# Performance work log

Measured on AMD Instinct MI355X. Metric: run time of the kernel, lower is better.

## Reference

```python
import jax, jax.numpy as jnp
import numpy as np
from jax import lax

N_IN = 200000
N_OUT = 400000
K3 = 27
M = 100000
C_IN = 128
C_OUT = 128
EPS = 1e-5


def setup_inputs() -> dict:
    key = jax.random.key(0)
    k1, k2, k3, k4 = jax.random.split(key, 4)
    feats = jax.random.normal(k1, (N_IN, C_IN), dtype=jnp.float32)
    W = jax.random.normal(k2, (K3, C_IN, C_OUT), dtype=jnp.float32) * (1.0 / np.sqrt(C_IN))
    gamma = jnp.ones((C_OUT,), dtype=jnp.float32)
    beta = jnp.zeros((C_OUT,), dtype=jnp.float32)
    in_maps = jax.random.randint(k3, (K3, M), 0, N_IN, dtype=jnp.int32)
    out_maps = jax.random.randint(k4, (K3, M), 0, N_OUT, dtype=jnp.int32)
    return {"feats": feats, "W": W, "gamma": gamma, "beta": beta,
            "in_maps": in_maps, "out_maps": out_maps, "n_out": N_OUT}


def sparse_conv_transpose(feats, W, in_maps, out_maps, n_out):
    # gather-GEMM-scatter over K3 kernel offsets (fixed small set -> scan)
    out0 = jnp.zeros((n_out, W.shape[-1]), dtype=feats.dtype)

    def body(out, xs):
        im, om, Wk = xs                      # [M], [M], [C_in, C_out]
        contrib = feats[im] @ Wk             # gather [M, C_in] -> GEMM -> [M, C_out]
        return out.at[om].add(contrib), None  # scatter-add

    out, _ = lax.scan(body, out0, (in_maps, out_maps, W))
    return out


def reference(feats, W, gamma, beta, in_maps, out_maps, n_out):
    out = sparse_conv_transpose(feats, W, in_maps, out_maps, n_out)  # [N_out, C_out]
    # MinkowskiBatchNorm (training mode): per-channel stats over all points
    mean = jnp.mean(out, axis=0)
    var = jnp.var(out, axis=0)
    y = (out - mean) * lax.rsqrt(var + EPS) * gamma + beta
    return y
```

## Files before the change

### kernel.cpp

```cpp
#include <hip/hip_runtime.h>

#define K3c    27
#define Mc     100000
#define NINc   200000
#define NOUTc  400000
#define Cc     128
#define EPSc   1e-5f

#define NBUCK  6250
#define NCNT   (K3c * NBUCK)
#define BPK    391
#define CPK    1563

#define WS_STATS   0u
#define WS_COUNTS  4096u
#define WS_SIM     1048576u
#define WS_SOM     12582912u
#define WS_WFH     25165824u
#define WS_WFL     26214400u

typedef __attribute__((ext_vector_type(8))) short short8;
typedef __attribute__((ext_vector_type(4))) float f32x4;

__device__ inline unsigned fbits(float f) { return __builtin_bit_cast(unsigned, f); }
__device__ inline float bfloat(unsigned u) { return __builtin_bit_cast(float, u); }

__device__ inline unsigned pack_hi2(float f0, float f1) {
    return (fbits(f0) >> 16) | (fbits(f1) & 0xFFFF0000u);
}
__device__ inline float trunc_bf16_f(float f) { return bfloat(fbits(f) & 0xFFFF0000u); }

__device__ inline unsigned short bf16_rne(float f) {
    unsigned u = fbits(f);
    u += 0x7FFFu + ((u >> 16) & 1u);
    return (unsigned short)(u >> 16);
}

__global__ __launch_bounds__(256) void zero_kernel(float4* __restrict__ out4,
                                                   float* __restrict__ ws_stats,
                                                   unsigned* __restrict__ counts) {
    const int n4 = NOUTc * (Cc / 4);
    const int stride = gridDim.x * blockDim.x;
    int idx = blockIdx.x * blockDim.x + threadIdx.x;
    const float4 z = make_float4(0.f, 0.f, 0.f, 0.f);
    for (int i = idx; i < n4; i += stride) out4[i] = z;
    for (int i = idx; i < NCNT; i += stride) counts[i] = 0u;
    if (idx < 512) ws_stats[idx] = 0.f;
}

__global__ __launch_bounds__(256) void wprep_kernel(const float* __restrict__ W,
                                                    short8* __restrict__ wfh,
                                                    short8* __restrict__ wfl) {
    int tid = blockIdx.x * 256 + threadIdx.x;
    int k     = tid >> 11;
    int rem   = tid & 2047;
    int kstep = rem >> 9;
    int cb    = (rem >> 6) & 7;
    int lane  = rem & 63;
    int n   = cb * 16 + (lane & 15);
    int kk0 = kstep * 32 + (lane >> 4) * 8;
    const float* src = W + k * (Cc * Cc) + kk0 * Cc + n;
    short8 h, l;
#pragma unroll
    for (int j = 0; j < 8; ++j) {
        float f = src[j * Cc];
        unsigned short hb = bf16_rne(f);
        h[j] = (short)hb;
        float hf = bfloat(((unsigned)hb) << 16);
        l[j] = (short)bf16_rne(f - hf);
    }
    wfh[tid] = h;
    wfl[tid] = l;
}

__global__ __launch_bounds__(256) void hist_kernel(const int* __restrict__ out_maps,
                                                   unsigned* __restrict__ counts) {
    int b = blockIdx.x;
    int k = b / BPK;
    int m = (b - k * BPK) * 256 + threadIdx.x;
    if (m < Mc) {
        int om = out_maps[k * Mc + m];
        atomicAdd(&counts[k * NBUCK + (om >> 6)], 1u);
    }
}

__global__ __launch_bounds__(1024) void scan_kernel(unsigned* __restrict__ counts) {
    __shared__ unsigned lds[1024];
    const int t = threadIdx.x;
    const int CHUNK = 165;
    int base = t * CHUNK;
    unsigned s = 0;
    for (int j = 0; j < CHUNK; ++j) {
        int i = base + j;
        if (i < NCNT) s += counts[i];
    }
    lds[t] = s;
    __syncthreads();
    for (int off = 1; off < 1024; off <<= 1) {
        unsigned v = (t >= off) ? lds[t - off] : 0u;
        __syncthreads();
        lds[t] += v;
        __syncthreads();
    }
    unsigned run = lds[t] - s;
    for (int j = 0; j < CHUNK; ++j) {
        int i = base + j;
        if (i < NCNT) {
            unsigned c = counts[i];
            counts[i] = run;
            run += c;
        }
    }
}

__global__ __launch_bounds__(256) void build_kernel(const int* __restrict__ in_maps,
                                                    const int* __restrict__ out_maps,
                                                    unsigned* __restrict__ offs,
                                                    int* __restrict__ sorted_im,
                                                    int* __restrict__ sorted_om) {
    int b = blockIdx.x;
    int k = b / BPK;
    int m = (b - k * BPK) * 256 + threadIdx.x;
    if (m < Mc) {
        int om = out_maps[k * Mc + m];
        int im = in_maps[k * Mc + m];
        unsigned pos = atomicAdd(&offs[k * NBUCK + (om >> 6)], 1u);
        sorted_im[pos] = im;
        sorted_om[pos] = om;
    }
}

__global__ __launch_bounds__(256) void gemm_scatter_kernel(
    const float* __restrict__ feats,
    const short8* __restrict__ wfh, const short8* __restrict__ wfl,
    const int* __restrict__ sorted_im, const int* __restrict__ sorted_om,
    float* __restrict__ out)
{
    __shared__ short fsh[64 * 136];
    __shared__ short fsl[64 * 136];

    const int t = threadIdx.x;
    const int bx = blockIdx.x;
    const int k = bx / CPK;
    const int c = bx - k * CPK;
    const int pairbase = k * Mc + c * 64;
    const int valid = min(64, Mc - c * 64);

    {
        const int r = t >> 2;
        const int cg = t & 3;
        const bool ok = (r < valid);
        long im = ok ? (long)sorted_im[pairbase + r] : 0;
        const float4* src4 = (const float4*)(feats + im * Cc + cg * 32);
        unsigned* fh32 = (unsigned*)fsh;
        unsigned* fl32 = (unsigned*)fsl;
#pragma unroll
        for (int j = 0; j < 8; ++j) {
            float4 v = ok ? src4[j] : make_float4(0.f, 0.f, 0.f, 0.f);
            int col = cg * 32 + j * 4;
            int idx = r * 68 + (col >> 1);
            fh32[idx]     = pack_hi2(v.x, v.y);
            fh32[idx + 1] = pack_hi2(v.z, v.w);
            float lx = v.x - trunc_bf16_f(v.x);
            float ly = v.y - trunc_bf16_f(v.y);
            float lz = v.z - trunc_bf16_f(v.z);
            float lw = v.w - trunc_bf16_f(v.w);
            fl32[idx]     = pack_hi2(lx, ly);
            fl32[idx + 1] = pack_hi2(lz, lw);
        }
    }
    __syncthreads();

    const int wave = t >> 6;
    const int lane = t & 63;
    const int m    = lane & 15;
    const int quad = lane >> 4;

    f32x4 acc[8];
#pragma unroll
    for (int cb = 0; cb < 8; ++cb) acc[cb] = (f32x4){0.f, 0.f, 0.f, 0.f};

    const int arow = wave * 16 + m;
    for (int kstep = 0; kstep < 4; ++kstep) {
        const short* ah = fsh + arow * 136 + kstep * 32 + quad * 8;
        const short* al = fsl + arow * 136 + kstep * 32 + quad * 8;
        short8 a_hi = *(const short8*)ah;
        short8 a_lo = *(const short8*)al;
        int fb = ((k * 4 + kstep) * 8) * 64 + lane;
#pragma unroll
        for (int cb = 0; cb < 8; ++cb) {
            short8 b_hi = wfh[fb + cb * 64];
            short8 b_lo = wfl[fb + cb * 64];
            acc[cb] = __builtin_amdgcn_mfma_f32_16x16x32_bf16(a_hi, b_hi, acc[cb], 0, 0, 0);
            acc[cb] = __builtin_amdgcn_mfma_f32_16x16x32_bf16(a_lo, b_hi, acc[cb], 0, 0, 0);
            acc[cb] = __builtin_amdgcn_mfma_f32_16x16x32_bf16(a_hi, b_lo, acc[cb], 0, 0, 0);
        }
    }

    const int rbase = wave * 16 + quad * 4;
#pragma unroll
    for (int reg = 0; reg < 4; ++reg) {
        int row = rbase + reg;
        if (row < valid) {
            long om = (long)sorted_om[pairbase + row];
            float* dst = out + om * Cc + m;
#pragma unroll
            for (int cb = 0; cb < 8; ++cb)
                unsafeAtomicAdd(dst + cb * 16, acc[cb][reg]);
        }
    }
}

__global__ __launch_bounds__(256) void stats_kernel(const float4* __restrict__ out4,
                                                    float* __restrict__ stats) {
    const int t  = threadIdx.x;
    const int tx = t & 31;
    const int ty = t >> 5;

    float4 s = make_float4(0.f, 0.f, 0.f, 0.f);
    float4 q = make_float4(0.f, 0.f, 0.f, 0.f);
    int row0 = blockIdx.x * 400 + ty;
    for (int j = 0; j < 50; ++j) {
        float4 v = out4[(row0 + j * 8) * 32 + tx];
        s.x += v.x; s.y += v.y; s.z += v.z; s.w += v.w;
        q.x += v.x * v.x; q.y += v.y * v.y; q.z += v.z * v.z; q.w += v.w * v.w;
    }

    __shared__ float4 redS[256];
    __shared__ float4 redQ[256];
    redS[t] = s; redQ[t] = q;
    __syncthreads();
    if (ty == 0) {
#pragma unroll
        for (int jj = 1; jj < 8; ++jj) {
            float4 o = redS[jj * 32 + tx];
            s.x += o.x; s.y += o.y; s.z += o.z; s.w += o.w;
            float4 oq = redQ[jj * 32 + tx];
            q.x += oq.x; q.y += oq.y; q.z += oq.z; q.w += oq.w;
        }
        unsafeAtomicAdd(&stats[tx * 4 + 0], s.x);
        unsafeAtomicAdd(&stats[tx * 4 + 1], s.y);
        unsafeAtomicAdd(&stats[tx * 4 + 2], s.z);
        unsafeAtomicAdd(&stats[tx * 4 + 3], s.w);
        unsafeAtomicAdd(&stats[Cc + tx * 4 + 0], q.x);
        unsafeAtomicAdd(&stats[Cc + tx * 4 + 1], q.y);
        unsafeAtomicAdd(&stats[Cc + tx * 4 + 2], q.z);
        unsafeAtomicAdd(&stats[Cc + tx * 4 + 3], q.w);
    }
}

__global__ void finalize_kernel(const float* __restrict__ gamma,
                                const float* __restrict__ beta,
                                float* __restrict__ stats) {
    int c = threadIdx.x;
    float inv_n = 1.0f / (float)NOUTc;
    float mean = stats[c] * inv_n;
    float var  = stats[Cc + c] * inv_n - mean * mean;
    float scale = gamma[c] * rsqrtf(var + EPSc);
    stats[2 * Cc + c] = scale;
    stats[3 * Cc + c] = beta[c] - mean * scale;
}

__global__ __launch_bounds__(256) void norm_kernel(float4* __restrict__ out4,
                                                   const float* __restrict__ stats) {
    const float4* stats4 = (const float4*)stats;
    int idx0 = blockIdx.x * blockDim.x + threadIdx.x;
    int c4 = idx0 & 31;
    float4 sc = stats4[64 + c4];
    float4 sh = stats4[96 + c4];
    const int n4 = NOUTc * (Cc / 4);
    const int stride = gridDim.x * blockDim.x;
    for (int i = idx0; i < n4; i += stride) {
        float4 v = out4[i];
        v.x = v.x * sc.x + sh.x;
        v.y = v.y * sc.y + sh.y;
        v.z = v.z * sc.z + sh.z;
        v.w = v.w * sc.w + sh.w;
        out4[i] = v;
    }
}

extern "C" void kernel_launch(void* const* d_in, const int* in_sizes, int n_in,
                              void* d_out, int out_size, void* d_ws, size_t ws_size,
                              hipStream_t stream) {
    const float* feats    = (const float*)d_in[0];
    const float* W        = (const float*)d_in[1];
    const float* gamma    = (const float*)d_in[2];
    const float* beta     = (const float*)d_in[3];
    const int*   in_maps  = (const int*)d_in[4];
    const int*   out_maps = (const int*)d_in[5];
    float* out = (float*)d_out;

    char* ws = (char*)d_ws;
    float*    stats     = (float*)(ws + WS_STATS);
    unsigned* counts    = (unsigned*)(ws + WS_COUNTS);
    int*      sorted_im = (int*)(ws + WS_SIM);
    int*      sorted_om = (int*)(ws + WS_SOM);
    short8*   wfh       = (short8*)(ws + WS_WFH);
    short8*   wfl       = (short8*)(ws + WS_WFL);

    zero_kernel<<<4096, 256, 0, stream>>>((float4*)out, stats, counts);
    wprep_kernel<<<216, 256, 0, stream>>>(W, wfh, wfl);
    hist_kernel<<<K3c * BPK, 256, 0, stream>>>(out_maps, counts);
    scan_kernel<<<1, 1024, 0, stream>>>(counts);
    build_kernel<<<K3c * BPK, 256, 0, stream>>>(in_maps, out_maps, counts,
                                                sorted_im, sorted_om);
    gemm_scatter_kernel<<<K3c * CPK, 256, 0, stream>>>(feats, wfh, wfl,
                                                       sorted_im, sorted_om, out);
    stats_kernel<<<1000, 256, 0, stream>>>((const float4*)out, stats);
    finalize_kernel<<<1, 128, 0, stream>>>(gamma, beta, stats);
    norm_kernel<<<4096, 256, 0, stream>>>((float4*)out, stats);
}
```

Baseline: 2.319 ms.

## Bucket pairs by output tile, accumulate in LDS, fuse stats into gemm

Reorders the counting-sort key to bucket-major (output tile of 64 rows, then kernel offset), so each block owns one 64-row output tile. All contributions for that tile accumulate via workgroup-scope LDS atomics, and the tile is written once. This removes the zeroing of the output, the global float atomics and the separate stats pass, which is folded into the block epilogue. Features are gathered straight from global memory into registers, and im, k and the row are packed into one 32-bit word. The cost is uneven per-block work, only 6250 blocks, and wave-level dynamic scheduling over the 27 offsets with partially filled 16-row MFMA tiles.

```diff
diff --git a/kernel.cpp b/kernel.cpp
--- a/kernel.cpp
+++ b/kernel.cpp
@@ -8,14 +8,12 @@
 #define EPSc   1e-5f
 
 #define NBUCK  6250
-#define NCNT   (K3c * NBUCK)
+#define NCNT   (NBUCK * K3c)
 #define BPK    391
-#define CPK    1563
 
 #define WS_STATS   0u
 #define WS_COUNTS  4096u
-#define WS_SIM     1048576u
-#define WS_SOM     12582912u
+#define WS_SPK     1048576u
 #define WS_WFH     25165824u
 #define WS_WFL     26214400u
 
@@ -24,11 +22,6 @@
 
 __device__ inline unsigned fbits(float f) { return __builtin_bit_cast(unsigned, f); }
 __device__ inline float bfloat(unsigned u) { return __builtin_bit_cast(float, u); }
-
-__device__ inline unsigned pack_hi2(float f0, float f1) {
-    return (fbits(f0) >> 16) | (fbits(f1) & 0xFFFF0000u);
-}
-__device__ inline float trunc_bf16_f(float f) { return bfloat(fbits(f) & 0xFFFF0000u); }
 
 __device__ inline unsigned short bf16_rne(float f) {
     unsigned u = fbits(f);
@@ -36,16 +29,15 @@
     return (unsigned short)(u >> 16);
 }
 
-__global__ __launch_bounds__(256) void zero_kernel(float4* __restrict__ out4,
-                                                   float* __restrict__ ws_stats,
-                                                   unsigned* __restrict__ counts) {
-    const int n4 = NOUTc * (Cc / 4);
-    const int stride = gridDim.x * blockDim.x;
-    int idx = blockIdx.x * blockDim.x + threadIdx.x;
-    const float4 z = make_float4(0.f, 0.f, 0.f, 0.f);
-    for (int i = idx; i < n4; i += stride) out4[i] = z;
-    for (int i = idx; i < NCNT; i += stride) counts[i] = 0u;
-    if (idx < 512) ws_stats[idx] = 0.f;
+#define SPLIT1(F, H, L) { unsigned hb_ = fbits(F) & 0xFFFF0000u; \
+                          (H) = (short)(hb_ >> 16); \
+                          (L) = (short)(fbits((F) - bfloat(hb_)) >> 16); }
+
+__global__ __launch_bounds__(256) void zero2_kernel(float* __restrict__ stats,
+                                                    unsigned* __restrict__ counts) {
+    int idx = blockIdx.x * 256 + threadIdx.x;
+    if (idx < NCNT) counts[idx] = 0u;
+    if (idx < 512) stats[idx] = 0.f;
 }
 
 __global__ __launch_bounds__(256) void wprep_kernel(const float* __restrict__ W,
@@ -73,14 +65,14 @@
     wfl[tid] = l;
 }
 
-__global__ __launch_bounds__(256) void hist_kernel(const int* __restrict__ out_maps,
-                                                   unsigned* __restrict__ counts) {
+__global__ __launch_bounds__(256) void hist2_kernel(const int* __restrict__ out_maps,
+                                                    unsigned* __restrict__ counts) {
     int b = blockIdx.x;
     int k = b / BPK;
     int m = (b - k * BPK) * 256 + threadIdx.x;
     if (m < Mc) {
         int om = out_maps[k * Mc + m];
-        atomicAdd(&counts[k * NBUCK + (om >> 6)], 1u);
+        atomicAdd(&counts[(unsigned)(om >> 6) * 27u + (unsigned)k], 1u);
     }
 }
 
@@ -113,139 +105,164 @@
     }
 }
 
-__global__ __launch_bounds__(256) void build_kernel(const int* __restrict__ in_maps,
-                                                    const int* __restrict__ out_maps,
-                                                    unsigned* __restrict__ offs,
-                                                    int* __restrict__ sorted_im,
-                                                    int* __restrict__ sorted_om) {
+__global__ __launch_bounds__(256) void build2_kernel(const int* __restrict__ in_maps,
+                                                     const int* __restrict__ out_maps,
+                                                     unsigned* __restrict__ offs,
+                                                     unsigned* __restrict__ sorted_pk) {
     int b = blockIdx.x;
     int k = b / BPK;
     int m = (b - k * BPK) * 256 + threadIdx.x;
     if (m < Mc) {
         int om = out_maps[k * Mc + m];
         int im = in_maps[k * Mc + m];
-        unsigned pos = atomicAdd(&offs[k * NBUCK + (om >> 6)], 1u);
-        sorted_im[pos] = im;
-        sorted_om[pos] = om;
-    }
-}
-
-__global__ __launch_bounds__(256) void gemm_scatter_kernel(
+        unsigned pos = atomicAdd(&offs[(unsigned)(om >> 6) * 27u + (unsigned)k], 1u);
+        sorted_pk[pos] = (unsigned)im | ((unsigned)k << 18) | ((unsigned)(om & 63) << 23);
+    }
+}
+
+__global__ __launch_bounds__(256, 4) void gemm2_kernel(
     const float* __restrict__ feats,
     const short8* __restrict__ wfh, const short8* __restrict__ wfl,
-    const int* __restrict__ sorted_im, const int* __restrict__ sorted_om,
-    float* __restrict__ out)
+    const unsigned* __restrict__ counts,
+    const unsigned* __restrict__ sorted_pk,
+    float* __restrict__ out, float* __restrict__ stats)
 {
-    __shared__ short fsh[64 * 136];
-    __shared__ short fsl[64 * 136];
-
+    __shared__ float accs[64 * Cc];
+    __shared__ unsigned earr[28];
+    __shared__ int kctr;
+    __shared__ float sred[Cc], qred[Cc];
+
+    const int b = blockIdx.x;
     const int t = threadIdx.x;
-    const int bx = blockIdx.x;
-    const int k = bx / CPK;
-    const int c = bx - k * CPK;
-    const int pairbase = k * Mc + c * 64;
-    const int valid = min(64, Mc - c * 64);
-
+
+    if (t < 27) earr[t + 1] = counts[b * 27 + t];
+    if (t == 27) earr[0] = (b == 0) ? 0u : counts[b * 27 - 1];
+    if (t == 28) kctr = 0;
     {
-        const int r = t >> 2;
-        const int cg = t & 3;
-        const bool ok = (r < valid);
-        long im = ok ? (long)sorted_im[pairbase + r] : 0;
-        const float4* src4 = (const float4*)(feats + im * Cc + cg * 32);
-        unsigned* fh32 = (unsigned*)fsh;
-        unsigned* fl32 = (unsigned*)fsl;
-#pragma unroll
-        for (int j = 0; j < 8; ++j) {
-            float4 v = ok ? src4[j] : make_float4(0.f, 0.f, 0.f, 0.f);
-            int col = cg * 32 + j * 4;
-            int idx = r * 68 + (col >> 1);
-            fh32[idx]     = pack_hi2(v.x, v.y);
-            fh32[idx + 1] = pack_hi2(v.z, v.w);
-            float lx = v.x - trunc_bf16_f(v.x);
-            float ly = v.y - trunc_bf16_f(v.y);
-            float lz = v.z - trunc_bf16_f(v.z);
-            float lw = v.w - trunc_bf16_f(v.w);
-            fl32[idx]     = pack_hi2(lx, ly);
-            fl32[idx + 1] = pack_hi2(lz, lw);
-        }
+        f32x4* a4 = (f32x4*)accs;
+        const f32x4 z = {0.f, 0.f, 0.f, 0.f};
+#pragma unroll
+        for (int i = 0; i < 8; ++i) a4[t + i * 256] = z;
     }
     __syncthreads();
 
-    const int wave = t >> 6;
     const int lane = t & 63;
     const int m    = lane & 15;
     const int quad = lane >> 4;
 
-    f32x4 acc[8];
-#pragma unroll
-    for (int cb = 0; cb < 8; ++cb) acc[cb] = (f32x4){0.f, 0.f, 0.f, 0.f};
-
-    const int arow = wave * 16 + m;
-    for (int kstep = 0; kstep < 4; ++kstep) {
-        const short* ah = fsh + arow * 136 + kstep * 32 + quad * 8;
-        const short* al = fsl + arow * 136 + kstep * 32 + quad * 8;
-        short8 a_hi = *(const short8*)ah;
-        short8 a_lo = *(const short8*)al;
-        int fb = ((k * 4 + kstep) * 8) * 64 + lane;
-#pragma unroll
-        for (int cb = 0; cb < 8; ++cb) {
-            short8 b_hi = wfh[fb + cb * 64];
-            short8 b_lo = wfl[fb + cb * 64];
-            acc[cb] = __builtin_amdgcn_mfma_f32_16x16x32_bf16(a_hi, b_hi, acc[cb], 0, 0, 0);
-            acc[cb] = __builtin_amdgcn_mfma_f32_16x16x32_bf16(a_lo, b_hi, acc[cb], 0, 0, 0);
-            acc[cb] = __builtin_amdgcn_mfma_f32_16x16x32_bf16(a_hi, b_lo, acc[cb], 0, 0, 0);
-        }
-    }
-
-    const int rbase = wave * 16 + quad * 4;
-#pragma unroll
-    for (int reg = 0; reg < 4; ++reg) {
-        int row = rbase + reg;
-        if (row < valid) {
-            long om = (long)sorted_om[pairbase + row];
-            float* dst = out + om * Cc + m;
-#pragma unroll
-            for (int cb = 0; cb < 8; ++cb)
-                unsafeAtomicAdd(dst + cb * 16, acc[cb][reg]);
-        }
-    }
-}
-
-__global__ __launch_bounds__(256) void stats_kernel(const float4* __restrict__ out4,
-                                                    float* __restrict__ stats) {
-    const int t  = threadIdx.x;
-    const int tx = t & 31;
-    const int ty = t >> 5;
-
-    float4 s = make_float4(0.f, 0.f, 0.f, 0.f);
-    float4 q = make_float4(0.f, 0.f, 0.f, 0.f);
-    int row0 = blockIdx.x * 400 + ty;
-    for (int j = 0; j < 50; ++j) {
-        float4 v = out4[(row0 + j * 8) * 32 + tx];
-        s.x += v.x; s.y += v.y; s.z += v.z; s.w += v.w;
-        q.x += v.x * v.x; q.y += v.y * v.y; q.z += v.z * v.z; q.w += v.w * v.w;
-    }
-
-    __shared__ float4 redS[256];
-    __shared__ float4 redQ[256];
-    redS[t] = s; redQ[t] = q;
+    for (;;) {
+        int kk = 0;
+        if (lane == 0) kk = atomicAdd(&kctr, 1);
+        kk = __shfl(kk, 0);
+        if (kk >= K3c) break;
+        const unsigned sk = earr[kk];
+        const unsigned ek = earr[kk + 1];
+        for (unsigned p0 = sk; p0 < ek; p0 += 32) {
+            const int nA = (int)(ek - p0);
+            const int n0 = nA < 16 ? nA : 16;
+            int n1 = nA - 16; n1 = n1 < 0 ? 0 : (n1 > 16 ? 16 : n1);
+            const bool two = (n1 > 0);
+
+            unsigned pk0 = (m < n0) ? sorted_pk[p0 + m] : 0u;
+            unsigned pk1 = (two && m < n1) ? sorted_pk[p0 + 16 + m] : 0u;
+            const float* ap0 = feats + (long)(pk0 & 0x3FFFFu) * Cc + quad * 8;
+            const float* ap1 = feats + (long)(pk1 & 0x3FFFFu) * Cc + quad * 8;
+
+            f32x4 acc0[8], acc1[8];
+            const f32x4 z = {0.f, 0.f, 0.f, 0.f};
+#pragma unroll
+            for (int cb = 0; cb < 8; ++cb) { acc0[cb] = z; acc1[cb] = z; }
+
+            for (int kstep = 0; kstep < 4; ++kstep) {
+                short8 a0h, a0l, a1h, a1l;
+                {
+                    float4 v0 = *(const float4*)(ap0 + kstep * 32);
+                    float4 v1 = *(const float4*)(ap0 + kstep * 32 + 4);
+                    SPLIT1(v0.x, a0h[0], a0l[0]); SPLIT1(v0.y, a0h[1], a0l[1]);
+                    SPLIT1(v0.z, a0h[2], a0l[2]); SPLIT1(v0.w, a0h[3], a0l[3]);
+                    SPLIT1(v1.x, a0h[4], a0l[4]); SPLIT1(v1.y, a0h[5], a0l[5]);
+                    SPLIT1(v1.z, a0h[6], a0l[6]); SPLIT1(v1.w, a0h[7], a0l[7]);
+                }
+                if (two) {
+                    float4 v0 = *(const float4*)(ap1 + kstep * 32);
+                    float4 v1 = *(const float4*)(ap1 + kstep * 32 + 4);
+                    SPLIT1(v0.x, a1h[0], a1l[0]); SPLIT1(v0.y, a1h[1], a1l[1]);
+                    SPLIT1(v0.z, a1h[2], a1l[2]); SPLIT1(v0.w, a1h[3], a1l[3]);
+                    SPLIT1(v1.x, a1h[4], a1l[4]); SPLIT1(v1.y, a1h[5], a1l[5]);
+                    SPLIT1(v1.z, a1h[6], a1l[6]); SPLIT1(v1.w, a1h[7], a1l[7]);
+                }
+                const int fb = ((kk * 4 + kstep) * 8) * 64 + lane;
+#pragma unroll
+                for (int cb = 0; cb < 8; ++cb) {
+                    short8 bh = wfh[fb + cb * 64];
+                    short8 bl = wfl[fb + cb * 64];
+                    acc0[cb] = __builtin_amdgcn_mfma_f32_16x16x32_bf16(a0h, bh, acc0[cb], 0, 0, 0);
+                    acc0[cb] = __builtin_amdgcn_mfma_f32_16x16x32_bf16(a0l, bh, acc0[cb], 0, 0, 0);
+                    acc0[cb] = __builtin_amdgcn_mfma_f32_16x16x32_bf16(a0h, bl, acc0[cb], 0, 0, 0);
+                    if (two) {
+                        acc1[cb] = __builtin_amdgcn_mfma_f32_16x16x32_bf16(a1h, bh, acc1[cb], 0, 0, 0);
+                        acc1[cb] = __builtin_amdgcn_mfma_f32_16x16x32_bf16(a1l, bh, acc1[cb], 0, 0, 0);
+                        acc1[cb] = __builtin_amdgcn_mfma_f32_16x16x32_bf16(a1h, bl, acc1[cb], 0, 0, 0);
+                    }
+                }
+            }
+
+#pragma unroll
+            for (int reg = 0; reg < 4; ++reg) {
+                const int prow = quad * 4 + reg;
+                unsigned pks = (unsigned)__shfl((int)pk0, prow);
+                if (prow < n0) {
+                    float* dst = accs + ((pks >> 23) & 63u) * Cc + m;
+#pragma unroll
+                    for (int cb = 0; cb < 8; ++cb)
+                        __hip_atomic_fetch_add(dst + cb * 16, acc0[cb][reg],
+                                               __ATOMIC_RELAXED, __HIP_MEMORY_SCOPE_WORKGROUP);
+                }
+            }
+            if (two) {
+#pragma unroll
+                for (int reg = 0; reg < 4; ++reg) {
+                    const int prow = quad * 4 + reg;
+                    unsigned pks = (unsigned)__shfl((int)pk1, prow);
+                    if (prow < n1) {
+                        float* dst = accs + ((pks >> 23) & 63u) * Cc + m;
+#pragma unroll
+                        for (int cb = 0; cb < 8; ++cb)
+                            __hip_atomic_fetch_add(dst + cb * 16, acc1[cb][reg],
+                                                   __ATOMIC_RELAXED, __HIP_MEMORY_SCOPE_WORKGROUP);
+                    }
+                }
+            }
+        }
+    }
     __syncthreads();
-    if (ty == 0) {
-#pragma unroll
-        for (int jj = 1; jj < 8; ++jj) {
-            float4 o = redS[jj * 32 + tx];
-            s.x += o.x; s.y += o.y; s.z += o.z; s.w += o.w;
-            float4 oq = redQ[jj * 32 + tx];
-            q.x += oq.x; q.y += oq.y; q.z += oq.z; q.w += oq.w;
-        }
-        unsafeAtomicAdd(&stats[tx * 4 + 0], s.x);
-        unsafeAtomicAdd(&stats[tx * 4 + 1], s.y);
-        unsafeAtomicAdd(&stats[tx * 4 + 2], s.z);
-        unsafeAtomicAdd(&stats[tx * 4 + 3], s.w);
-        unsafeAtomicAdd(&stats[Cc + tx * 4 + 0], q.x);
-        unsafeAtomicAdd(&stats[Cc + tx * 4 + 1], q.y);
-        unsafeAtomicAdd(&stats[Cc + tx * 4 + 2], q.z);
-        unsafeAtomicAdd(&stats[Cc + tx * 4 + 3], q.w);
+
+    {
+        const int c4 = t & 31;
+        const int rg = t >> 5;
+        float4* dst4 = (float4*)(out + (long)b * 64 * Cc);
+        const float4* a4 = (const float4*)accs;
+#pragma unroll
+        for (int i = 0; i < 8; ++i) {
+            const int r = rg * 8 + i;
+            dst4[r * 32 + c4] = a4[r * 32 + c4];
+        }
+    }
+    {
+        const int col  = t & 127;
+        const int half = t >> 7;
+        float s = 0.f, q = 0.f;
+        for (int r = half * 32; r < half * 32 + 32; ++r) {
+            float v = accs[r * Cc + col];
+            s += v; q += v * v;
+        }
+        if (half) { sred[col] = s; qred[col] = q; }
+        __syncthreads();
+        if (!half) {
+            s += sred[col]; q += qred[col];
+            unsafeAtomicAdd(&stats[col], s);
+            unsafeAtomicAdd(&stats[Cc + col], q);
+        }
     }
 }
 
@@ -294,20 +311,16 @@
     char* ws = (char*)d_ws;
     float*    stats     = (float*)(ws + WS_STATS);
     unsigned* counts    = (unsigned*)(ws + WS_COUNTS);
-    int*      sorted_im = (int*)(ws + WS_SIM);
-    int*      sorted_om = (int*)(ws + WS_SOM);
+    unsigned* sorted_pk = (unsigned*)(ws + WS_SPK);
     short8*   wfh       = (short8*)(ws + WS_WFH);
     short8*   wfl       = (short8*)(ws + WS_WFL);
 
-    zero_kernel<<<4096, 256, 0, stream>>>((float4*)out, stats, counts);
+    zero2_kernel<<<660, 256, 0, stream>>>(stats, counts);
     wprep_kernel<<<216, 256, 0, stream>>>(W, wfh, wfl);
-    hist_kernel<<<K3c * BPK, 256, 0, stream>>>(out_maps, counts);
+    hist2_kernel<<<K3c * BPK, 256, 0, stream>>>(out_maps, counts);
     scan_kernel<<<1, 1024, 0, stream>>>(counts);
-    build_kernel<<<K3c * BPK, 256, 0, stream>>>(in_maps, out_maps, counts,
-                                                sorted_im, sorted_om);
-    gemm_scatter_kernel<<<K3c * CPK, 256, 0, stream>>>(feats, wfh, wfl,
-                                                       sorted_im, sorted_om, out);
-    stats_kernel<<<1000, 256, 0, stream>>>((const float4*)out, stats);
+    build2_kernel<<<K3c * BPK, 256, 0, stream>>>(in_maps, out_maps, counts, sorted_pk);
+    gemm2_kernel<<<NBUCK, 256, 0, stream>>>(feats, wfh, wfl, counts, sorted_pk, out, stats);
     finalize_kernel<<<1, 128, 0, stream>>>(gamma, beta, stats);
     norm_kernel<<<4096, 256, 0, stream>>>((float4*)out, stats);
 }
```

Measured after the change: 2.784 ms. 1.2x slower.

## Replace atomic scatter-add with sorted contribution buffer and per-output segmented reduction

Applied to the files above, without the earlier changes.

The GEMM kernel now writes each row's contribution to a slot in a staging buffer, using a second counting sort keyed by output row. A separate kernel then sums each output row's contributions and writes the result with plain stores. This removes the float atomics into the output and the full zeroing of the output. In exchange it adds a global histogram and scan over 400k rows, extra staging traffic (fp16 when workspace is small, which loses precision), and work split into slabs with many more launches.

```diff
diff --git a/kernel.cpp b/kernel.cpp
--- a/kernel.cpp
+++ b/kernel.cpp
@@ -1,4 +1,5 @@
 #include <hip/hip_runtime.h>
+#include <hip/hip_fp16.h>
 
 #define K3c    27
 #define Mc     100000
@@ -8,16 +9,22 @@
 #define EPSc   1e-5f
 
 #define NBUCK  6250
-#define NCNT   (K3c * NBUCK)
+#define NCNTA  (K3c * NBUCK)
+#define NCNTG  NOUTc
 #define BPK    391
-#define CPK    1563
+#define SCANBA 165
+#define SCANBG 391
 
 #define WS_STATS   0u
-#define WS_COUNTS  4096u
-#define WS_SIM     1048576u
-#define WS_SOM     12582912u
-#define WS_WFH     25165824u
-#define WS_WFL     26214400u
+#define WS_CNTA    4096u
+#define WS_AUXA    679936u
+#define WS_CNTG    681984u
+#define WS_AUXG    2282496u
+#define WS_WFH     2285568u
+#define WS_WFL     3170304u
+#define WS_SIMA    4055040u
+#define WS_PGA     14855040u
+#define WS_CBUF    25657344u
 
 typedef __attribute__((ext_vector_type(8))) short short8;
 typedef __attribute__((ext_vector_type(4))) float f32x4;
@@ -36,16 +43,19 @@
     return (unsigned short)(u >> 16);
 }
 
-__global__ __launch_bounds__(256) void zero_kernel(float4* __restrict__ out4,
-                                                   float* __restrict__ ws_stats,
-                                                   unsigned* __restrict__ counts) {
-    const int n4 = NOUTc * (Cc / 4);
-    const int stride = gridDim.x * blockDim.x;
-    int idx = blockIdx.x * blockDim.x + threadIdx.x;
-    const float4 z = make_float4(0.f, 0.f, 0.f, 0.f);
-    for (int i = idx; i < n4; i += stride) out4[i] = z;
-    for (int i = idx; i < NCNT; i += stride) counts[i] = 0u;
-    if (idx < 512) ws_stats[idx] = 0.f;
+__device__ inline unsigned short f2h(float f) { return __half_as_ushort(__float2half(f)); }
+__device__ inline float h2f(unsigned short u) { return __half2float(__ushort_as_half(u)); }
+
+__device__ inline void storeC(unsigned short* p, float v) { *p = f2h(v); }
+__device__ inline void storeC(float* p, float v) { *p = v; }
+
+__global__ __launch_bounds__(256) void zero3_kernel(float* __restrict__ stats,
+                                                    unsigned* __restrict__ cntA,
+                                                    unsigned* __restrict__ cntG) {
+    int idx = blockIdx.x * 256 + threadIdx.x;
+    if (idx < NCNTA) cntA[idx] = 0u;
+    if (idx < NCNTG) cntG[idx] = 0u;
+    if (idx < 512) stats[idx] = 0.f;
 }
 
 __global__ __launch_bounds__(256) void wprep_kernel(const float* __restrict__ W,
@@ -73,84 +83,107 @@
     wfl[tid] = l;
 }
 
-__global__ __launch_bounds__(256) void hist_kernel(const int* __restrict__ out_maps,
-                                                   unsigned* __restrict__ counts) {
+__global__ __launch_bounds__(256) void hist3_kernel(const int* __restrict__ out_maps,
+                                                    unsigned* __restrict__ cntA,
+                                                    unsigned* __restrict__ cntG) {
     int b = blockIdx.x;
     int k = b / BPK;
     int m = (b - k * BPK) * 256 + threadIdx.x;
     if (m < Mc) {
         int om = out_maps[k * Mc + m];
-        atomicAdd(&counts[k * NBUCK + (om >> 6)], 1u);
-    }
-}
-
-__global__ __launch_bounds__(1024) void scan_kernel(unsigned* __restrict__ counts) {
+        atomicAdd(&cntA[k * NBUCK + (om >> 6)], 1u);
+        atomicAdd(&cntG[om], 1u);
+    }
+}
+
+__global__ __launch_bounds__(1024) void scan_a(unsigned* __restrict__ c,
+                                               unsigned* __restrict__ aux, int n) {
     __shared__ unsigned lds[1024];
     const int t = threadIdx.x;
-    const int CHUNK = 165;
-    int base = t * CHUNK;
-    unsigned s = 0;
-    for (int j = 0; j < CHUNK; ++j) {
-        int i = base + j;
-        if (i < NCNT) s += counts[i];
-    }
-    lds[t] = s;
+    const int i = blockIdx.x * 1024 + t;
+    unsigned v = (i < n) ? c[i] : 0u;
+    lds[t] = v;
     __syncthreads();
     for (int off = 1; off < 1024; off <<= 1) {
-        unsigned v = (t >= off) ? lds[t - off] : 0u;
+        unsigned x = (t >= off) ? lds[t - off] : 0u;
         __syncthreads();
-        lds[t] += v;
+        lds[t] += x;
         __syncthreads();
     }
-    unsigned run = lds[t] - s;
-    for (int j = 0; j < CHUNK; ++j) {
-        int i = base + j;
-        if (i < NCNT) {
-            unsigned c = counts[i];
-            counts[i] = run;
-            run += c;
-        }
-    }
-}
-
-__global__ __launch_bounds__(256) void build_kernel(const int* __restrict__ in_maps,
-                                                    const int* __restrict__ out_maps,
-                                                    unsigned* __restrict__ offs,
-                                                    int* __restrict__ sorted_im,
-                                                    int* __restrict__ sorted_om) {
+    if (i < n) c[i] = lds[t] - v;
+    if (t == 1023) aux[blockIdx.x] = lds[1023];
+}
+
+__global__ __launch_bounds__(1024) void scan_b(unsigned* __restrict__ aux, int nb) {
+    __shared__ unsigned lds[1024];
+    const int t = threadIdx.x;
+    unsigned v = (t < nb) ? aux[t] : 0u;
+    lds[t] = v;
+    __syncthreads();
+    for (int off = 1; off < 1024; off <<= 1) {
+        unsigned x = (t >= off) ? lds[t - off] : 0u;
+        __syncthreads();
+        lds[t] += x;
+        __syncthreads();
+    }
+    if (t < nb) aux[t] = lds[t] - v;
+}
+
+__global__ __launch_bounds__(1024) void scan_c(unsigned* __restrict__ c,
+                                               const unsigned* __restrict__ aux, int n) {
+    const int i = blockIdx.x * 1024 + threadIdx.x;
+    if (i < n) c[i] += aux[blockIdx.x];
+}
+
+__global__ __launch_bounds__(256) void build3_kernel(const int* __restrict__ in_maps,
+                                                     const int* __restrict__ out_maps,
+                                                     unsigned* __restrict__ cntA,
+                                                     unsigned* __restrict__ cntG,
+                                                     int* __restrict__ simA,
+                                                     unsigned* __restrict__ pgA) {
     int b = blockIdx.x;
     int k = b / BPK;
     int m = (b - k * BPK) * 256 + threadIdx.x;
     if (m < Mc) {
         int om = out_maps[k * Mc + m];
         int im = in_maps[k * Mc + m];
-        unsigned pos = atomicAdd(&offs[k * NBUCK + (om >> 6)], 1u);
-        sorted_im[pos] = im;
-        sorted_om[pos] = om;
-    }
-}
-
-__global__ __launch_bounds__(256) void gemm_scatter_kernel(
+        unsigned posA = atomicAdd(&cntA[k * NBUCK + (om >> 6)], 1u);
+        unsigned posG = atomicAdd(&cntG[om], 1u);
+        simA[posA] = im;
+        pgA[posA]  = posG;
+    }
+}
+
+template <typename ST>
+__global__ __launch_bounds__(256) void phaseA_kernel(
     const float* __restrict__ feats,
     const short8* __restrict__ wfh, const short8* __restrict__ wfl,
-    const int* __restrict__ sorted_im, const int* __restrict__ sorted_om,
-    float* __restrict__ out)
+    const unsigned* __restrict__ endA,
+    const unsigned* __restrict__ endG,
+    const int* __restrict__ simA, const unsigned* __restrict__ pgA,
+    ST* __restrict__ cbuf, int B0, int B1, int CPSL, unsigned capRows)
 {
     __shared__ short fsh[64 * 136];
     __shared__ short fsl[64 * 136];
-
-    const int t = threadIdx.x;
+    __shared__ unsigned posr[64];
+
+    const int t  = threadIdx.x;
     const int bx = blockIdx.x;
-    const int k = bx / CPK;
-    const int c = bx - k * CPK;
-    const int pairbase = k * Mc + c * 64;
-    const int valid = min(64, Mc - c * 64);
+    const int k  = bx / CPSL;
+    const int ci = bx - k * CPSL;
+    const unsigned lo = (k == 0 && B0 == 0) ? 0u : endA[k * NBUCK + B0 - 1];
+    const unsigned hi = endA[k * NBUCK + B1 - 1];
+    const unsigned start = lo + (unsigned)ci * 64u;
+    if (start >= hi) return;
+    const int valid = (int)(hi - start < 64u ? hi - start : 64u);
+    const unsigned slabBase = (B0 == 0) ? 0u : endG[B0 * 64 - 1];
 
     {
-        const int r = t >> 2;
+        const int r  = t >> 2;
         const int cg = t & 3;
         const bool ok = (r < valid);
-        long im = ok ? (long)sorted_im[pairbase + r] : 0;
+        long im = ok ? (long)simA[start + r] : 0;
+        if (cg == 0) posr[r] = ok ? (pgA[start + r] - slabBase) : 0xFFFFFFFFu;
         const float4* src4 = (const float4*)(feats + im * Cc + cg * 32);
         unsigned* fh32 = (unsigned*)fsh;
         unsigned* fl32 = (unsigned*)fsl;
@@ -202,13 +235,65 @@
     for (int reg = 0; reg < 4; ++reg) {
         int row = rbase + reg;
         if (row < valid) {
-            long om = (long)sorted_om[pairbase + row];
-            float* dst = out + om * Cc + m;
-#pragma unroll
-            for (int cb = 0; cb < 8; ++cb)
-                unsafeAtomicAdd(dst + cb * 16, acc[cb][reg]);
-        }
-    }
+            unsigned rp = posr[row];
+            if (rp < capRows) {
+                ST* dst = cbuf + (size_t)rp * Cc + m;
+#pragma unroll
+                for (int cb = 0; cb < 8; ++cb)
+                    storeC(dst + cb * 16, acc[cb][reg]);
+            }
+        }
+    }
+}
+
+template <typename ST>
+__global__ __launch_bounds__(256) void phaseB_kernel(
+    const ST* __restrict__ cbuf, const unsigned* __restrict__ endG,
+    float* __restrict__ out, int B0)
+{
+    __shared__ unsigned ends[66];
+    const int t = threadIdx.x;
+    const int bucket = B0 + blockIdx.x;
+    const int om0 = bucket * 64;
+    if (t < 65) ends[t] = (om0 + t == 0) ? 0u : endG[om0 + t - 1];
+    if (t == 65) ends[65] = (B0 == 0) ? 0u : endG[B0 * 64 - 1];
+    __syncthreads();
+    const unsigned sbase = ends[65];
+    const int r  = t >> 2;
+    const int cg = t & 3;
+    unsigned e0 = ends[r] - sbase;
+    unsigned e1 = ends[r + 1] - sbase;
+
+    float a[32];
+#pragma unroll
+    for (int j = 0; j < 32; ++j) a[j] = 0.f;
+
+    for (unsigned e = e0; e < e1; ++e) {
+        const ST* src = cbuf + (size_t)e * Cc + cg * 32;
+        if constexpr (sizeof(ST) == 2) {
+            const short8* s8 = (const short8*)src;
+#pragma unroll
+            for (int p = 0; p < 4; ++p) {
+                short8 v = s8[p];
+#pragma unroll
+                for (int j = 0; j < 8; ++j)
+                    a[p * 8 + j] += h2f((unsigned short)v[j]);
+            }
+        } else {
+            const float4* f4 = (const float4*)src;
+#pragma unroll
+            for (int p = 0; p < 8; ++p) {
+                float4 v = f4[p];
+                a[p * 4 + 0] += v.x; a[p * 4 + 1] += v.y;
+                a[p * 4 + 2] += v.z; a[p * 4 + 3] += v.w;
+            }
+        }
+    }
+
+    float4* dst = (float4*)(out + (size_t)(om0 + r) * Cc + cg * 32);
+#pragma unroll
+    for (int p = 0; p < 8; ++p)
+        dst[p] = make_float4(a[p * 4], a[p * 4 + 1], a[p * 4 + 2], a[p * 4 + 3]);
 }
 
 __global__ __launch_bounds__(256) void stats_kernel(const float4* __restrict__ out4,
@@ -292,21 +377,62 @@
     float* out = (float*)d_out;
 
     char* ws = (char*)d_ws;
-    float*    stats     = (float*)(ws + WS_STATS);
-    unsigned* counts    = (unsigned*)(ws + WS_COUNTS);
-    int*      sorted_im = (int*)(ws + WS_SIM);
-    int*      sorted_om = (int*)(ws + WS_SOM);
-    short8*   wfh       = (short8*)(ws + WS_WFH);
-    short8*   wfl       = (short8*)(ws + WS_WFL);
-
-    zero_kernel<<<4096, 256, 0, stream>>>((float4*)out, stats, counts);
+    float*    stats = (float*)(ws + WS_STATS);
+    unsigned* cntA  = (unsigned*)(ws + WS_CNTA);
+    unsigned* auxA  = (unsigned*)(ws + WS_AUXA);
+    unsigned* cntG  = (unsigned*)(ws + WS_CNTG);
+    unsigned* auxG  = (unsigned*)(ws + WS_AUXG);
+    short8*   wfh   = (short8*)(ws + WS_WFH);
+    short8*   wfl   = (short8*)(ws + WS_WFL);
+    int*      simA  = (int*)(ws + WS_SIMA);
+    unsigned* pgA   = (unsigned*)(ws + WS_PGA);
+
+    zero3_kernel<<<1563, 256, 0, stream>>>(stats, cntA, cntG);
     wprep_kernel<<<216, 256, 0, stream>>>(W, wfh, wfl);
-    hist_kernel<<<K3c * BPK, 256, 0, stream>>>(out_maps, counts);
-    scan_kernel<<<1, 1024, 0, stream>>>(counts);
-    build_kernel<<<K3c * BPK, 256, 0, stream>>>(in_maps, out_maps, counts,
-                                                sorted_im, sorted_om);
-    gemm_scatter_kernel<<<K3c * CPK, 256, 0, stream>>>(feats, wfh, wfl,
-                                                       sorted_im, sorted_om, out);
+    hist3_kernel<<<K3c * BPK, 256, 0, stream>>>(out_maps, cntA, cntG);
+    scan_a<<<SCANBA, 1024, 0, stream>>>(cntA, auxA, NCNTA);
+    scan_b<<<1, 1024, 0, stream>>>(auxA, SCANBA);
+    scan_c<<<SCANBA, 1024, 0, stream>>>(cntA, auxA, NCNTA);
+    scan_a<<<SCANBG, 1024, 0, stream>>>(cntG, auxG, NCNTG);
+    scan_b<<<1, 1024, 0, stream>>>(auxG, SCANBG);
+    scan_c<<<SCANBG, 1024, 0, stream>>>(cntG, auxG, NCNTG);
+    build3_kernel<<<K3c * BPK, 256, 0, stream>>>(in_maps, out_maps, cntA, cntG,
+                                                 simA, pgA);
+
+    size_t cap = (ws_size > WS_CBUF) ? (size_t)(ws_size - WS_CBUF) : 0;
+    auto slabs_for = [&](size_t eb) -> int {
+        for (int n = 1; n <= 64; ++n) {
+            double rows = 2700000.0 / n * 1.04 + 4096.0;
+            if ((size_t)rows * 128ull * eb <= cap) return n;
+        }
+        return -1;
+    };
+    int n32 = slabs_for(4);
+    int n16 = slabs_for(2);
+    bool use_f32 = (n32 > 0 && n32 <= 8);
+    int nslab = use_f32 ? n32 : (n16 > 0 ? n16 : 64);
+    const int SB = (NBUCK + nslab - 1) / nslab;
+    const int CPSL = (int)(16.0 * SB * 1.10 / 64.0) + 3;
+
+    for (int s = 0; s < nslab; ++s) {
+        int B0 = s * SB;
+        int B1 = (B0 + SB < NBUCK) ? B0 + SB : NBUCK;
+        if (B0 >= B1) break;
+        if (use_f32) {
+            unsigned capRows = (unsigned)(cap / (128ull * 4ull));
+            float* cbuf = (float*)(ws + WS_CBUF);
+            phaseA_kernel<float><<<K3c * CPSL, 256, 0, stream>>>(
+                feats, wfh, wfl, cntA, cntG, simA, pgA, cbuf, B0, B1, CPSL, capRows);
+            phaseB_kernel<float><<<B1 - B0, 256, 0, stream>>>(cbuf, cntG, out, B0);
+        } else {
+            unsigned capRows = (unsigned)(cap / (128ull * 2ull));
+            unsigned short* cbuf = (unsigned short*)(ws + WS_CBUF);
+            phaseA_kernel<unsigned short><<<K3c * CPSL, 256, 0, stream>>>(
+                feats, wfh, wfl, cntA, cntG, simA, pgA, cbuf, B0, B1, CPSL, capRows);
+            phaseB_kernel<unsigned short><<<B1 - B0, 256, 0, stream>>>(cbuf, cntG, out, B0);
+        }
+    }
+
     stats_kernel<<<1000, 256, 0, stream>>>((const float4*)out, stats);
     finalize_kernel<<<1, 128, 0, stream>>>(gamma, beta, stats);
     norm_kernel<<<4096, 256, 0, stream>>>((float4*)out, stats);
```

After: 2.515 ms. 1.08x slower.
